# Optimization experiments

Measured on AMD Instinct MI355X. Metric: run time of the kernel, lower is better.

The kernel has to match this reference:

```python
import jax, jax.numpy as jnp
import numpy as np

# Module config (matches init_kwargs)
H, W, C = 32, 32, 256
K = 3                      # filter_size
B = 16
TEMP = 1.0                 # softmax_temp
CH, CW = H - K + 1, W - K + 1   # convs_height/width (valid padding, stride 1)
NF = CH * CW               # num_convs
FS = K * K                 # filter_size squared (window size)
HW = H * W


def _local_indices():
    # flattened (row-major over H,W) positions of each KxK window, sorted ascending
    idx = np.zeros((NF, FS), dtype=np.int32)
    c = 0
    for i in range(CH):
        for j in range(CW):
            win = [(i + di) * W + (j + dj) for di in range(K) for dj in range(K)]
            idx[c] = np.sort(win)
            c += 1
    return jnp.asarray(idx)


def setup_inputs() -> dict:
    key = jax.random.key(0)
    ks = jax.random.split(key, 7)
    s = 1.0 / np.sqrt(C)  # torch Linear default init scale
    return {
        "batch": jax.random.normal(ks[0], (B, C, H, W), dtype=jnp.float32),
        "key_w": jax.random.uniform(ks[1], (C, C), jnp.float32, -s, s),
        "key_b": jax.random.uniform(ks[2], (C,), jnp.float32, -s, s),
        "query_w": jax.random.uniform(ks[3], (C, C), jnp.float32, -s, s),
        "query_b": jax.random.uniform(ks[4], (C,), jnp.float32, -s, s),
        "value_w": jax.random.uniform(ks[5], (1, C), jnp.float32, -s, s),
        "value_b": jax.random.uniform(ks[6], (1,), jnp.float32, -s, s),
        "local_indices": _local_indices(),
    }


def _normalize(t):
    # F.normalize(dim=-1), eps=1e-12
    return t / jnp.maximum(jnp.linalg.norm(t, axis=-1, keepdims=True), 1e-12)


def reference(batch, key_w, key_b, query_w, query_b, value_w, value_b, local_indices):
    # [B,C,H,W] -> [B,HW,C]
    x = batch.transpose(0, 2, 3, 1).reshape(B, HW, C)
    # local patches: X_l[f,b,k,c] = x[b, local_indices[f,k], c]  -> [NF,B,FS,C]
    X_l = x[:, local_indices].transpose(1, 0, 2, 3)
    # global is the full (unmasked) feature map: X_g = x  -> [B,HW,C]
    keys = x @ key_w.T + key_b                       # [B,HW,C]
    queries = X_l @ query_w.T + query_b              # [NF,B,FS,C]
    values = (x @ value_w.T + value_b)[..., 0]       # [B,HW]
    # cosine similarity: [NF,B,HW,FS]
    comp = jnp.einsum('bnc,fbkc->fbnk', _normalize(keys), _normalize(queries))
    att = jax.nn.softmax(TEMP * comp, axis=2)        # softmax over HW
    # W_g[f,b,k] = sum_n values[b,n] * att[f,b,n,k]
    W_g = jnp.einsum('bn,fbnk->fbk', values, att)
    # convolved: sum over window positions, weighted
    conv = jnp.einsum('fbk,fbkc->fbc', W_g, X_l)     # [NF,B,C]
    out = conv.transpose(1, 0, 2).reshape(B, CH, CW, C).transpose(0, 3, 1, 2)
    return out  # [B,C,CH,CW]
```

## Files before the change

### kernel.cpp

```cpp
#include <hip/hip_runtime.h>
#include <hip/hip_bf16.h>


#define NB 16
#define NC 256
#define NHW 1024
#define NCH 30

typedef __attribute__((ext_vector_type(8))) short short8;
typedef __attribute__((ext_vector_type(4))) float f32x4;

static __device__ __forceinline__ unsigned short f2bf(float f) {
    __hip_bfloat16 h = __float2bfloat16(f);
    return *(unsigned short*)&h;
}
static __device__ __forceinline__ float bf2f(unsigned short u) {
    unsigned int x = ((unsigned int)u) << 16;
    return __uint_as_float(x);
}

__global__ __launch_bounds__(256) void wconv_kernel(
    const float* __restrict__ key_w, const float* __restrict__ query_w,
    unsigned short* __restrict__ kpk, unsigned short* __restrict__ qpk)
{
    const int gx = blockIdx.x;
    const int mat = gx >> 3, g = gx & 7, t = threadIdx.x;
    const float* src = mat ? query_w : key_w;
    unsigned short* dst = mat ? qpk : kpk;
    #pragma unroll
    for (int it = 0; it < 4; ++it) {
        int idx = it * 256 + t;
        int ct = idx >> 6, lane = idx & 63;
        int l15 = lane & 15, q = lane >> 4;
        const float* s = src + (ct * 16 + l15) * NC + g * 32 + q * 8;
        float4 a = *(const float4*)s;
        float4 c = *(const float4*)(s + 4);
        short8 o;
        o[0] = (short)f2bf(a.x); o[1] = (short)f2bf(a.y);
        o[2] = (short)f2bf(a.z); o[3] = (short)f2bf(a.w);
        o[4] = (short)f2bf(c.x); o[5] = (short)f2bf(c.y);
        o[6] = (short)f2bf(c.z); o[7] = (short)f2bf(c.w);
        *(short8*)(dst + ((size_t)(g * 16 + ct) * 64 + lane) * 8) = o;
    }
}

__global__ __launch_bounds__(512, 3) void fused_lin_kernel(
    const float* __restrict__ batch,
    const float* __restrict__ value_w, const float* __restrict__ value_b,
    const unsigned short* __restrict__ kpk, const unsigned short* __restrict__ qpk,
    const float* __restrict__ key_b, const float* __restrict__ query_b,
    unsigned short* __restrict__ xc,
    unsigned short* __restrict__ Kn, unsigned short* __restrict__ Qn,
    float* __restrict__ vout)
{
    const int b = blockIdx.y, n0 = blockIdx.x * 32;
    const int t = threadIdx.x, wave = t >> 6, lane = t & 63;
    const int l15 = lane & 15, quad = lane >> 4;

    __shared__ unsigned short Xs[2][32][72];
    __shared__ float PK[8][2][16], PQ[8][2][16];
    __shared__ float4 vred[8][8];

    const int c_l = t >> 3;
    const int n4  = (t & 7) * 4;
    const float* bb = batch + (size_t)b * NC * NHW + n0;
    unsigned short* xcp = xc + (size_t)b * NC * NHW + n0;
    float4 vacc = {0.f, 0.f, 0.f, 0.f};

    const unsigned short* kbase = kpk + (size_t)(wave * 2) * 512 + lane * 8;
    const unsigned short* qbase = qpk + (size_t)(wave * 2) * 512 + lane * 8;

    short8 wK[2][2], wQ[2][2];
    #pragma unroll
    for (int ct = 0; ct < 2; ++ct) {
        wK[0][ct] = *(const short8*)(kbase + ct * 512);
        wQ[0][ct] = *(const short8*)(qbase + ct * 512);
    }

    {
        float4 x0 = *(const float4*)(bb + (size_t)c_l * NHW + n4);
        ushort4 o0;
        o0.x = f2bf(x0.x); o0.y = f2bf(x0.y); o0.z = f2bf(x0.z); o0.w = f2bf(x0.w);
        *(ushort4*)(xcp + (size_t)c_l * NHW + n4) = o0;
        float w0 = value_w[c_l];
        vacc.x += x0.x * w0; vacc.y += x0.y * w0;
        vacc.z += x0.z * w0; vacc.w += x0.w * w0;
        Xs[0][n4 + 0][c_l] = o0.x; Xs[0][n4 + 1][c_l] = o0.y;
        Xs[0][n4 + 2][c_l] = o0.z; Xs[0][n4 + 3][c_l] = o0.w;
    }
    __syncthreads();

    f32x4 accK[2][2], accQ[2][2];
    #pragma unroll
    for (int ct = 0; ct < 2; ++ct) {
        int co = wave * 32 + ct * 16 + l15;
        float bK = key_b[co], bQ = query_b[co];
        accK[0][ct] = (f32x4){bK, bK, bK, bK};
        accK[1][ct] = (f32x4){bK, bK, bK, bK};
        accQ[0][ct] = (f32x4){bQ, bQ, bQ, bQ};
        accQ[1][ct] = (f32x4){bQ, bQ, bQ, bQ};
    }

    for (int cc = 0; cc < 4; ++cc) {
        float4 x_pf;
        if (cc < 3)
            x_pf = *(const float4*)(bb + (size_t)((cc + 1) * 64 + c_l) * NHW + n4);

        const int cur = cc & 1;
        #pragma unroll
        for (int kc = 0; kc < 2; ++kc) {
            const int g = cc * 2 + kc;
            if (g < 7) {
                const int nb_ = (g + 1) & 1;
                #pragma unroll
                for (int ct = 0; ct < 2; ++ct) {
                    wK[nb_][ct] = *(const short8*)(kbase + (g + 1) * 8192 + ct * 512);
                    wQ[nb_][ct] = *(const short8*)(qbase + (g + 1) * 8192 + ct * 512);
                }
            }
            short8 af0 = *(const short8*)&Xs[cur][l15][kc * 32 + quad * 8];
            short8 af1 = *(const short8*)&Xs[cur][16 + l15][kc * 32 + quad * 8];
            const int cb = g & 1;
            #pragma unroll
            for (int ct = 0; ct < 2; ++ct) {
                accK[0][ct] = __builtin_amdgcn_mfma_f32_16x16x32_bf16(af0, wK[cb][ct], accK[0][ct], 0, 0, 0);
                accK[1][ct] = __builtin_amdgcn_mfma_f32_16x16x32_bf16(af1, wK[cb][ct], accK[1][ct], 0, 0, 0);
                accQ[0][ct] = __builtin_amdgcn_mfma_f32_16x16x32_bf16(af0, wQ[cb][ct], accQ[0][ct], 0, 0, 0);
                accQ[1][ct] = __builtin_amdgcn_mfma_f32_16x16x32_bf16(af1, wQ[cb][ct], accQ[1][ct], 0, 0, 0);
            }
        }

        if (cc < 3) {
            int c0 = (cc + 1) * 64 + c_l;
            ushort4 o0;
            o0.x = f2bf(x_pf.x); o0.y = f2bf(x_pf.y);
            o0.z = f2bf(x_pf.z); o0.w = f2bf(x_pf.w);
            *(ushort4*)(xcp + (size_t)c0 * NHW + n4) = o0;
            float w0 = value_w[c0];
            vacc.x += x_pf.x * w0; vacc.y += x_pf.y * w0;
            vacc.z += x_pf.z * w0; vacc.w += x_pf.w * w0;
            const int nxt = (cc + 1) & 1;
            Xs[nxt][n4 + 0][c_l] = o0.x; Xs[nxt][n4 + 1][c_l] = o0.y;
            Xs[nxt][n4 + 2][c_l] = o0.z; Xs[nxt][n4 + 3][c_l] = o0.w;
            __syncthreads();
        }
    }

    #pragma unroll
    for (int o = 8; o <= 32; o <<= 1) {
        vacc.x += __shfl_xor(vacc.x, o, 64); vacc.y += __shfl_xor(vacc.y, o, 64);
        vacc.z += __shfl_xor(vacc.z, o, 64); vacc.w += __shfl_xor(vacc.w, o, 64);
    }

    float nK[2][4] = {{0, 0, 0, 0}, {0, 0, 0, 0}};
    float nQ[2][4] = {{0, 0, 0, 0}, {0, 0, 0, 0}};
    #pragma unroll
    for (int ns = 0; ns < 2; ++ns)
        #pragma unroll
        for (int ct = 0; ct < 2; ++ct)
            #pragma unroll
            for (int r = 0; r < 4; ++r) {
                nK[ns][r] += accK[ns][ct][r] * accK[ns][ct][r];
                nQ[ns][r] += accQ[ns][ct][r] * accQ[ns][ct][r];
            }
    #pragma unroll
    for (int ns = 0; ns < 2; ++ns)
        #pragma unroll
        for (int r = 0; r < 4; ++r)
            #pragma unroll
            for (int o = 1; o < 16; o <<= 1) {
                nK[ns][r] += __shfl_xor(nK[ns][r], o, 64);
                nQ[ns][r] += __shfl_xor(nQ[ns][r], o, 64);
            }
    if (l15 == 0)
        #pragma unroll
        for (int ns = 0; ns < 2; ++ns)
            #pragma unroll
            for (int r = 0; r < 4; ++r) {
                PK[wave][ns][quad * 4 + r] = nK[ns][r];
                PQ[wave][ns][quad * 4 + r] = nQ[ns][r];
            }
    if (lane < 8) vred[wave][lane] = vacc;
    __syncthreads();

    float ik[2][4], iq[2][4];
    #pragma unroll
    for (int ns = 0; ns < 2; ++ns)
        #pragma unroll
        for (int r = 0; r < 4; ++r) {
            int qr = quad * 4 + r;
            float sk = 0.f, sq = 0.f;
            #pragma unroll
            for (int w = 0; w < 8; ++w) { sk += PK[w][ns][qr]; sq += PQ[w][ns][qr]; }
            ik[ns][r] = 1.f / fmaxf(sqrtf(sk), 1e-12f);
            iq[ns][r] = 1.f / fmaxf(sqrtf(sq), 1e-12f);
        }
    #pragma unroll
    for (int ns = 0; ns < 2; ++ns)
        #pragma unroll
        for (int ct = 0; ct < 2; ++ct)
            #pragma unroll
            for (int r = 0; r < 4; ++r) {
                size_t row = (size_t)(b * NHW + n0 + ns * 16 + quad * 4 + r) * NC
                           + wave * 32 + ct * 16 + l15;
                Kn[row] = f2bf(accK[ns][ct][r] * ik[ns][r]);
                Qn[row] = f2bf(accQ[ns][ct][r] * iq[ns][r]);
            }
    if (t < 8) {
        float4 s = {0.f, 0.f, 0.f, 0.f};
        #pragma unroll
        for (int w = 0; w < 8; ++w) {
            float4 p = vred[w][t];
            s.x += p.x; s.y += p.y; s.z += p.z; s.w += p.w;
        }
        float vb = value_b[0];
        s.x += vb; s.y += vb; s.z += vb; s.w += vb;
        *(float4*)(vout + b * NHW + n0 + t * 4) = s;
    }
}

__global__ __launch_bounds__(512) void attn_kernel(
    const unsigned short* __restrict__ Kn,
    const unsigned short* __restrict__ Qn,
    const float* __restrict__ vbuf,
    float* __restrict__ R)
{
    const int b = blockIdx.y, m0 = blockIdx.x * 64;
    const int t = threadIdx.x, wave = t >> 6, lane = t & 63;
    const int l15 = lane & 15, quad = lane >> 4;

    short8 bf[4][8];
    #pragma unroll
    for (int ms = 0; ms < 4; ++ms) {
        const short* q = (const short*)Qn
                       + (size_t)(b * NHW + m0 + ms * 16 + l15) * NC + quad * 8;
        #pragma unroll
        for (int c = 0; c < 8; ++c) bf[ms][c] = *(const short8*)(q + 32 * c);
    }
    const float* vb = vbuf + b * NHW;
    const int nstart = wave * 128;
    const short* ka = (const short*)Kn + (size_t)(b * NHW + nstart + l15) * NC + quad * 8;

    float z[4] = {0.f, 0.f, 0.f, 0.f}, tc[4] = {0.f, 0.f, 0.f, 0.f};
    for (int it = 0; it < 8; ++it, ka += 16 * NC) {
        short8 af[8];
        #pragma unroll
        for (int c = 0; c < 8; ++c) af[c] = *(const short8*)(ka + 32 * c);
        f32x4 a0[4], a1[4];
        #pragma unroll
        for (int ms = 0; ms < 4; ++ms) { a0[ms] = (f32x4){0,0,0,0}; a1[ms] = (f32x4){0,0,0,0}; }
        #pragma unroll
        for (int c = 0; c < 4; ++c)
            #pragma unroll
            for (int ms = 0; ms < 4; ++ms) {
                a0[ms] = __builtin_amdgcn_mfma_f32_16x16x32_bf16(af[c],     bf[ms][c],     a0[ms], 0, 0, 0);
                a1[ms] = __builtin_amdgcn_mfma_f32_16x16x32_bf16(af[c + 4], bf[ms][c + 4], a1[ms], 0, 0, 0);
            }
        float4 vv = *(const float4*)(vb + nstart + it * 16 + quad * 4);
        #pragma unroll
        for (int ms = 0; ms < 4; ++ms)
            #pragma unroll
            for (int r = 0; r < 4; ++r) {
                float e = __expf(a0[ms][r] + a1[ms][r]);
                z[ms] += e;
                tc[ms] += ((const float*)&vv)[r] * e;
            }
    }
    #pragma unroll
    for (int ms = 0; ms < 4; ++ms) {
        z[ms]  += __shfl_xor(z[ms], 16, 64);  z[ms]  += __shfl_xor(z[ms], 32, 64);
        tc[ms] += __shfl_xor(tc[ms], 16, 64); tc[ms] += __shfl_xor(tc[ms], 32, 64);
    }

    __shared__ float zs[8][4][16], ts[8][4][16];
    if (lane < 16)
        #pragma unroll
        for (int ms = 0; ms < 4; ++ms) {
            zs[wave][ms][l15] = z[ms];
            ts[wave][ms][l15] = tc[ms];
        }
    __syncthreads();
    if (t < 64) {
        int ms = t >> 4, li = t & 15;
        float zz = 0.f, tt = 0.f;
        #pragma unroll
        for (int w = 0; w < 8; ++w) { zz += zs[w][ms][li]; tt += ts[w][ms][li]; }
        R[b * NHW + m0 + ms * 16 + li] = tt / zz;
    }
}

__global__ __launch_bounds__(256) void out_kernel(
    const unsigned short* __restrict__ xc,
    const float* __restrict__ R,
    float* __restrict__ out)
{
    const int bc = blockIdx.x;
    const int b  = bc >> 8;
    const int t  = threadIdx.x;
    __shared__ float P[NHW];

    const unsigned short* xp = xc + (size_t)bc * NHW;
    const float* rp = R + b * NHW;
    {
        ushort4 xv = *(const ushort4*)(xp + t * 4);
        float4  rv = *(const float4*)(rp + t * 4);
        P[t * 4 + 0] = rv.x * bf2f(xv.x);
        P[t * 4 + 1] = rv.y * bf2f(xv.y);
        P[t * 4 + 2] = rv.z * bf2f(xv.z);
        P[t * 4 + 3] = rv.w * bf2f(xv.w);
    }
    __syncthreads();
    for (int idx = t; idx < NCH * NCH; idx += 256) {
        int i = idx / NCH, j = idx - i * NCH;
        const float* pr = &P[i * 32 + j];
        float s = pr[0]  + pr[1]  + pr[2]
                + pr[32] + pr[33] + pr[34]
                + pr[64] + pr[65] + pr[66];
        out[(size_t)bc * (NCH * NCH) + idx] = s;
    }
}

extern "C" void kernel_launch(void* const* d_in, const int* in_sizes, int n_in,
                              void* d_out, int out_size, void* d_ws, size_t ws_size,
                              hipStream_t stream) {
    const float* batch   = (const float*)d_in[0];
    const float* key_w   = (const float*)d_in[1];
    const float* key_b   = (const float*)d_in[2];
    const float* query_w = (const float*)d_in[3];
    const float* query_b = (const float*)d_in[4];
    const float* value_w = (const float*)d_in[5];
    const float* value_b = (const float*)d_in[6];
    float* out = (float*)d_out;

    char* ws = (char*)d_ws;
    const size_t KQ = (size_t)NB * NHW * NC;
    unsigned short* xc  = (unsigned short*)ws;
    unsigned short* Kn  = xc + KQ;
    unsigned short* Qn  = Kn + KQ;
    unsigned short* kpk = Qn + KQ;
    unsigned short* qpk = kpk + NC * NC;
    float* vbuf = (float*)(qpk + NC * NC);
    float* Rbuf = vbuf + NB * NHW;

    wconv_kernel<<<16, 256, 0, stream>>>(key_w, query_w, kpk, qpk);
    fused_lin_kernel<<<dim3(32, NB), 512, 0, stream>>>(batch, value_w, value_b,
                                                       kpk, qpk, key_b, query_b,
                                                       xc, Kn, Qn, vbuf);
    attn_kernel<<<dim3(16, NB), 512, 0, stream>>>(Kn, Qn, vbuf, Rbuf);
    out_kernel<<<NB * NC, 256, 0, stream>>>(xc, Rbuf, out);
}
```

Before: 127.5 us.

## Load full channel tile upfront and deepen weight prefetch in fused linear kernel

All four 64-channel slices of the input tile are loaded at once into a single full-width LDS buffer, replacing the double-buffered per-slice loop and removing three block barriers. The MFMA loop is fully unrolled with weights prefetched two steps ahead through a triple buffer. The launch-bounds occupancy hint rises from 3 to 4 blocks per CU. In exchange the kernel uses more LDS per block and more registers for the extra buffers, which may fight the higher occupancy target or cause spills.

```diff
diff --git a/kernel.cpp b/kernel.cpp
--- a/kernel.cpp
+++ b/kernel.cpp
@@ -44,7 +44,7 @@
     }
 }
 
-__global__ __launch_bounds__(512, 3) void fused_lin_kernel(
+__global__ __launch_bounds__(512, 4) void fused_lin_kernel(
     const float* __restrict__ batch,
     const float* __restrict__ value_w, const float* __restrict__ value_b,
     const unsigned short* __restrict__ kpk, const unsigned short* __restrict__ qpk,
@@ -57,7 +57,7 @@
     const int t = threadIdx.x, wave = t >> 6, lane = t & 63;
     const int l15 = lane & 15, quad = lane >> 4;
 
-    __shared__ unsigned short Xs[2][32][72];
+    __shared__ unsigned short Xs[32][264];
     __shared__ float PK[8][2][16], PQ[8][2][16];
     __shared__ float4 vred[8][8];
 
@@ -67,27 +67,41 @@
     unsigned short* xcp = xc + (size_t)b * NC * NHW + n0;
     float4 vacc = {0.f, 0.f, 0.f, 0.f};
 
+    float4 xs0 = *(const float4*)(bb + (size_t)(c_l      ) * NHW + n4);
+    float4 xs1 = *(const float4*)(bb + (size_t)(c_l +  64) * NHW + n4);
+    float4 xs2 = *(const float4*)(bb + (size_t)(c_l + 128) * NHW + n4);
+    float4 xs3 = *(const float4*)(bb + (size_t)(c_l + 192) * NHW + n4);
+
     const unsigned short* kbase = kpk + (size_t)(wave * 2) * 512 + lane * 8;
     const unsigned short* qbase = qpk + (size_t)(wave * 2) * 512 + lane * 8;
 
-    short8 wK[2][2], wQ[2][2];
+    short8 wK[3][2], wQ[3][2];
     #pragma unroll
     for (int ct = 0; ct < 2; ++ct) {
         wK[0][ct] = *(const short8*)(kbase + ct * 512);
         wQ[0][ct] = *(const short8*)(qbase + ct * 512);
-    }
-
-    {
-        float4 x0 = *(const float4*)(bb + (size_t)c_l * NHW + n4);
-        ushort4 o0;
-        o0.x = f2bf(x0.x); o0.y = f2bf(x0.y); o0.z = f2bf(x0.z); o0.w = f2bf(x0.w);
-        *(ushort4*)(xcp + (size_t)c_l * NHW + n4) = o0;
-        float w0 = value_w[c_l];
-        vacc.x += x0.x * w0; vacc.y += x0.y * w0;
-        vacc.z += x0.z * w0; vacc.w += x0.w * w0;
-        Xs[0][n4 + 0][c_l] = o0.x; Xs[0][n4 + 1][c_l] = o0.y;
-        Xs[0][n4 + 2][c_l] = o0.z; Xs[0][n4 + 3][c_l] = o0.w;
-    }
+        wK[1][ct] = *(const short8*)(kbase + 8192 + ct * 512);
+        wQ[1][ct] = *(const short8*)(qbase + 8192 + ct * 512);
+    }
+
+    #define CONSUME(XS, CI)                                                  \
+    {                                                                        \
+        int c0 = (CI) + c_l;                                                 \
+        ushort4 o0;                                                          \
+        o0.x = f2bf(XS.x); o0.y = f2bf(XS.y);                                \
+        o0.z = f2bf(XS.z); o0.w = f2bf(XS.w);                                \
+        *(ushort4*)(xcp + (size_t)c0 * NHW + n4) = o0;                       \
+        float w0 = value_w[c0];                                              \
+        vacc.x += XS.x * w0; vacc.y += XS.y * w0;                            \
+        vacc.z += XS.z * w0; vacc.w += XS.w * w0;                            \
+        Xs[n4 + 0][c0] = o0.x; Xs[n4 + 1][c0] = o0.y;                        \
+        Xs[n4 + 2][c0] = o0.z; Xs[n4 + 3][c0] = o0.w;                        \
+    }
+    CONSUME(xs0, 0)
+    CONSUME(xs1, 64)
+    CONSUME(xs2, 128)
+    CONSUME(xs3, 192)
+    #undef CONSUME
     __syncthreads();
 
     f32x4 accK[2][2], accQ[2][2];
@@ -101,48 +115,25 @@
         accQ[1][ct] = (f32x4){bQ, bQ, bQ, bQ};
     }
 
-    for (int cc = 0; cc < 4; ++cc) {
-        float4 x_pf;
-        if (cc < 3)
-            x_pf = *(const float4*)(bb + (size_t)((cc + 1) * 64 + c_l) * NHW + n4);
-
-        const int cur = cc & 1;
-        #pragma unroll
-        for (int kc = 0; kc < 2; ++kc) {
-            const int g = cc * 2 + kc;
-            if (g < 7) {
-                const int nb_ = (g + 1) & 1;
-                #pragma unroll
-                for (int ct = 0; ct < 2; ++ct) {
-                    wK[nb_][ct] = *(const short8*)(kbase + (g + 1) * 8192 + ct * 512);
-                    wQ[nb_][ct] = *(const short8*)(qbase + (g + 1) * 8192 + ct * 512);
-                }
-            }
-            short8 af0 = *(const short8*)&Xs[cur][l15][kc * 32 + quad * 8];
-            short8 af1 = *(const short8*)&Xs[cur][16 + l15][kc * 32 + quad * 8];
-            const int cb = g & 1;
+    #pragma unroll
+    for (int g = 0; g < 8; ++g) {
+        if (g < 6) {
+            const int nb_ = (g + 2) % 3;
             #pragma unroll
             for (int ct = 0; ct < 2; ++ct) {
-                accK[0][ct] = __builtin_amdgcn_mfma_f32_16x16x32_bf16(af0, wK[cb][ct], accK[0][ct], 0, 0, 0);
-                accK[1][ct] = __builtin_amdgcn_mfma_f32_16x16x32_bf16(af1, wK[cb][ct], accK[1][ct], 0, 0, 0);
-                accQ[0][ct] = __builtin_amdgcn_mfma_f32_16x16x32_bf16(af0, wQ[cb][ct], accQ[0][ct], 0, 0, 0);
-                accQ[1][ct] = __builtin_amdgcn_mfma_f32_16x16x32_bf16(af1, wQ[cb][ct], accQ[1][ct], 0, 0, 0);
-            }
-        }
-
-        if (cc < 3) {
-            int c0 = (cc + 1) * 64 + c_l;
-            ushort4 o0;
-            o0.x = f2bf(x_pf.x); o0.y = f2bf(x_pf.y);
-            o0.z = f2bf(x_pf.z); o0.w = f2bf(x_pf.w);
-            *(ushort4*)(xcp + (size_t)c0 * NHW + n4) = o0;
-            float w0 = value_w[c0];
-            vacc.x += x_pf.x * w0; vacc.y += x_pf.y * w0;
-            vacc.z += x_pf.z * w0; vacc.w += x_pf.w * w0;
-            const int nxt = (cc + 1) & 1;
-            Xs[nxt][n4 + 0][c_l] = o0.x; Xs[nxt][n4 + 1][c_l] = o0.y;
-            Xs[nxt][n4 + 2][c_l] = o0.z; Xs[nxt][n4 + 3][c_l] = o0.w;
-            __syncthreads();
+                wK[nb_][ct] = *(const short8*)(kbase + (g + 2) * 8192 + ct * 512);
+                wQ[nb_][ct] = *(const short8*)(qbase + (g + 2) * 8192 + ct * 512);
+            }
+        }
+        short8 af0 = *(const short8*)&Xs[l15][g * 32 + quad * 8];
+        short8 af1 = *(const short8*)&Xs[16 + l15][g * 32 + quad * 8];
+        const int cb = g % 3;
+        #pragma unroll
+        for (int ct = 0; ct < 2; ++ct) {
+            accK[0][ct] = __builtin_amdgcn_mfma_f32_16x16x32_bf16(af0, wK[cb][ct], accK[0][ct], 0, 0, 0);
+            accK[1][ct] = __builtin_amdgcn_mfma_f32_16x16x32_bf16(af1, wK[cb][ct], accK[1][ct], 0, 0, 0);
+            accQ[0][ct] = __builtin_amdgcn_mfma_f32_16x16x32_bf16(af0, wQ[cb][ct], accQ[0][ct], 0, 0, 0);
+            accQ[1][ct] = __builtin_amdgcn_mfma_f32_16x16x32_bf16(af1, wQ[cb][ct], accQ[1][ct], 0, 0, 0);
         }
     }
 
```

New measurement: 128.2 us. About the same (+0.6%).
